# Kernel optimization log

Measured on AMD Instinct MI355X. Metric: run time of the kernel, lower is better.

The kernel has to match this reference:

```python
import jax, jax.numpy as jnp
import numpy as np

KEY_DIM = 1024
SCALE = KEY_DIM ** -0.5


def setup_inputs() -> dict:
    key = jax.random.key(0)
    k1, k2, k3, k4 = jax.random.split(key, 4)
    B, S, E = 4, 2048, 1024
    x = jax.random.normal(k1, (B, S, E), dtype=jnp.float32)
    WQ = jax.random.normal(k2, (KEY_DIM, E), dtype=jnp.float32) * (E ** -0.5)
    WK = jax.random.normal(k3, (KEY_DIM, E), dtype=jnp.float32) * (E ** -0.5)
    WV = jax.random.normal(k4, (KEY_DIM, E), dtype=jnp.float32) * (E ** -0.5)
    return {"x": x, "WQ": WQ, "WK": WK, "WV": WV}


def reference(x, WQ, WK, WV):
    # x: [B, S, E]; Linear(bias=False) weights are [out, in] as in torch.
    q = jnp.einsum('bse,ke->bsk', x, WQ)   # [B, S, K]
    k = jnp.einsum('bse,ke->bsk', x, WK)   # [B, S, K]
    v = jnp.einsum('bse,ve->bsv', x, WV)   # [B, S, V]
    scores = jnp.einsum('bsk,btk->bst', q, k) * SCALE  # [B, S, S]
    # Faithful to torch: mask where tril(scores) == 0 (upper triangle).
    masked = jnp.where(jnp.tril(scores) == 0, -jnp.inf, scores)
    attn = jax.nn.softmax(masked, axis=-1)
    return jnp.einsum('bst,btv->bsv', attn, v)  # dropout=0.0 -> identity
```

## Files before the change

kernel.cpp:

```cpp
#include <hip/hip_runtime.h>

typedef _Float16 f16x8 __attribute__((ext_vector_type(8)));
typedef unsigned short u16x8v __attribute__((ext_vector_type(8)));
typedef unsigned short u16x4v __attribute__((ext_vector_type(4)));
typedef float f32x4 __attribute__((ext_vector_type(4)));

constexpr int SEQ = 2048;
constexpr int DIM = 1024;
constexpr int BATCH = 4;
constexpr size_t NBS = (size_t)BATCH * SEQ * DIM;

static __device__ __forceinline__ unsigned short f2h(float f) {
    return __builtin_bit_cast(unsigned short, (_Float16)f);
}
static __device__ __forceinline__ float h2f(unsigned short u) {
    return (float)__builtin_bit_cast(_Float16, u);
}
static __device__ __forceinline__ f16x8 ldsld(const unsigned short* p) {
    return __builtin_bit_cast(f16x8, *(const u16x8v*)p);
}
static __device__ __forceinline__ void gld_lds16(const unsigned short* g, unsigned short* l) {
    __builtin_amdgcn_global_load_lds(
        (const __attribute__((address_space(1))) void*)g,
        (__attribute__((address_space(3))) void*)l, 16, 0, 0);
}

__global__ __launch_bounds__(256) void cvt_all(
    const float* __restrict__ X,
    const float* __restrict__ W0, const float* __restrict__ W1,
    const float* __restrict__ W2,
    unsigned short* __restrict__ Xf, unsigned short* __restrict__ Wf)
{
    const int b = blockIdx.x;
    const float* src;
    unsigned short* dst;
    int i;
    if (b < 8192) {
        src = X; dst = Xf;
        i = b * 256 + threadIdx.x;
    } else {
        const int wb = b - 8192;
        const int z = wb >> 10;
        src = (z == 0) ? W0 : (z == 1) ? W1 : W2;
        dst = Wf + (size_t)z * DIM * DIM;
        i = (wb & 1023) * 256 + threadIdx.x;
    }
    float4 f = ((const float4*)src)[i];
    u16x4v h;
    h.x = f2h(f.x); h.y = f2h(f.y); h.z = f2h(f.z); h.w = f2h(f.w);
    ((u16x4v*)dst)[i] = h;
}


__global__ __launch_bounds__(256) void qkv_gemm(
    const unsigned short* __restrict__ Xf, const unsigned short* __restrict__ Wf,
    unsigned short* __restrict__ Qf, unsigned short* __restrict__ Kf,
    unsigned short* __restrict__ Vt)
{
    __shared__ __attribute__((aligned(16))) unsigned short Ah[128 * 64];
    __shared__ __attribute__((aligned(16))) unsigned short Bh[128 * 64];
    const int m0 = blockIdx.x * 128, n0 = blockIdx.y * 128, z = blockIdx.z;
    const unsigned short* Wz = Wf + (size_t)z * DIM * DIM;
    const int tid = threadIdx.x;
    const int w = tid >> 6, lane = tid & 63, q = lane >> 4, c = lane & 15;
    const int wrow = (w >> 1) * 64, wcol = (w & 1) * 64;
    const int g8 = lane >> 3;
    const int cu = (lane & 7) ^ g8;
    const int srow = w * 8 + g8;
    const int scol = cu * 8;
    unsigned short* lA = Ah + w * 512;
    unsigned short* lB = Bh + w * 512;
    const int c7 = c & 7;

    f32x4 acc[4][4];
#pragma unroll
    for (int a = 0; a < 4; ++a)
#pragma unroll
        for (int b = 0; b < 4; ++b) acc[a][b] = (f32x4){0.f, 0.f, 0.f, 0.f};

    for (int k0 = 0; k0 < DIM; k0 += 64) {
        __syncthreads();
        {
            const size_t ga = (size_t)(m0 + srow) * DIM + k0 + scol;
            const size_t gb = (size_t)(n0 + srow) * DIM + k0 + scol;
#pragma unroll
            for (int j = 0; j < 4; ++j) {
                gld_lds16(Xf + ga + (size_t)(j * 32) * DIM, lA + j * 2048);
                gld_lds16(Wz + gb + (size_t)(j * 32) * DIM, lB + j * 2048);
            }
        }
        __syncthreads();
#pragma unroll
        for (int kk = 0; kk < 2; ++kk) {
            f16x8 ah[4], bh[4];
#pragma unroll
            for (int mi = 0; mi < 4; ++mi)
                ah[mi] = ldsld(Ah + (wrow + mi * 16 + c) * 64 + (((kk << 2) + q) ^ c7) * 8);
#pragma unroll
            for (int ni = 0; ni < 4; ++ni)
                bh[ni] = ldsld(Bh + (wcol + ni * 16 + c) * 64 + (((kk << 2) + q) ^ c7) * 8);
#pragma unroll
            for (int mi = 0; mi < 4; ++mi)
#pragma unroll
                for (int ni = 0; ni < 4; ++ni)
                    acc[mi][ni] = __builtin_amdgcn_mfma_f32_16x16x32_f16(ah[mi], bh[ni], acc[mi][ni], 0, 0, 0);
        }
    }

    if (z == 2) {
#pragma unroll
        for (int mi = 0; mi < 4; ++mi) {
            const int mg = m0 + wrow + mi * 16 + q * 4;
            const int bb = mg >> 11, ss = mg & (SEQ - 1);
#pragma unroll
            for (int ni = 0; ni < 4; ++ni) {
                const int col = n0 + wcol + ni * 16 + c;
                u16x4v v;
                v.x = f2h(acc[mi][ni][0]);
                v.y = f2h(acc[mi][ni][1]);
                v.z = f2h(acc[mi][ni][2]);
                v.w = f2h(acc[mi][ni][3]);
                *(u16x4v*)(Vt + ((size_t)bb * DIM + col) * SEQ + ss) = v;
            }
        }
    } else {
        unsigned short* OH = z ? Kf : Qf;
#pragma unroll
        for (int mi = 0; mi < 4; ++mi)
#pragma unroll
            for (int ni = 0; ni < 4; ++ni) {
                const int col = n0 + wcol + ni * 16 + c;
#pragma unroll
                for (int r = 0; r < 4; ++r) {
                    const int row = m0 + wrow + mi * 16 + q * 4 + r;
                    OH[(size_t)row * DIM + col] = f2h(acc[mi][ni][r]);
                }
            }
    }
}

__global__ __launch_bounds__(256) void scores_gemm1b(
    const unsigned short* __restrict__ Q, const unsigned short* __restrict__ K,
    unsigned short* __restrict__ S)
{
    if (blockIdx.y > blockIdx.x) return;
    __shared__ __attribute__((aligned(16))) unsigned short Ah[128 * 64];
    __shared__ __attribute__((aligned(16))) unsigned short Bh[128 * 64];
    const int i0 = blockIdx.x * 128, j0 = blockIdx.y * 128, b = blockIdx.z;
    const unsigned short* Qb = Q + (size_t)b * SEQ * DIM;
    const unsigned short* Kb = K + (size_t)b * SEQ * DIM;
    unsigned short* Sb = S + (size_t)b * SEQ * SEQ;
    const int tid = threadIdx.x;
    const int w = tid >> 6, lane = tid & 63, q = lane >> 4, c = lane & 15;
    const int wrow = (w >> 1) * 64, wcol = (w & 1) * 64;
    const int g8 = lane >> 3;
    const int cu = (lane & 7) ^ g8;
    const int srow = w * 8 + g8;
    const int scol = cu * 8;
    unsigned short* lA = Ah + w * 512;
    unsigned short* lB = Bh + w * 512;
    const int c7 = c & 7;

    f32x4 acc[4][4];
#pragma unroll
    for (int a = 0; a < 4; ++a)
#pragma unroll
        for (int bq = 0; bq < 4; ++bq) acc[a][bq] = (f32x4){0.f, 0.f, 0.f, 0.f};

    for (int k0 = 0; k0 < DIM; k0 += 64) {
        __syncthreads();
        {
            const size_t ga = (size_t)(i0 + srow) * DIM + k0 + scol;
            const size_t gb = (size_t)(j0 + srow) * DIM + k0 + scol;
#pragma unroll
            for (int j = 0; j < 4; ++j) {
                gld_lds16(Qb + ga + (size_t)(j * 32) * DIM, lA + j * 2048);
                gld_lds16(Kb + gb + (size_t)(j * 32) * DIM, lB + j * 2048);
            }
        }
        __syncthreads();
#pragma unroll
        for (int kk = 0; kk < 2; ++kk) {
            f16x8 ah[4], bh[4];
#pragma unroll
            for (int mi = 0; mi < 4; ++mi)
                ah[mi] = ldsld(Ah + (wrow + mi * 16 + c) * 64 + (((kk << 2) + q) ^ c7) * 8);
#pragma unroll
            for (int ni = 0; ni < 4; ++ni)
                bh[ni] = ldsld(Bh + (wcol + ni * 16 + c) * 64 + (((kk << 2) + q) ^ c7) * 8);
#pragma unroll
            for (int mi = 0; mi < 4; ++mi)
#pragma unroll
                for (int ni = 0; ni < 4; ++ni)
                    acc[mi][ni] = __builtin_amdgcn_mfma_f32_16x16x32_f16(ah[mi], bh[ni], acc[mi][ni], 0, 0, 0);
        }
    }
#pragma unroll
    for (int mi = 0; mi < 4; ++mi)
#pragma unroll
        for (int ni = 0; ni < 4; ++ni) {
            const int col = j0 + wcol + ni * 16 + c;
#pragma unroll
            for (int r = 0; r < 4; ++r) {
                const int row = i0 + wrow + mi * 16 + q * 4 + r;
                const float sc = acc[mi][ni][r] * 0.03125f;
                Sb[(size_t)row * SEQ + col] =
                    (sc == 0.f) ? (unsigned short)0xFC00u : f2h(sc);
            }
        }
}

__global__ __launch_bounds__(256) void softmax_row_b(
    const unsigned short* __restrict__ S, unsigned short* __restrict__ P)
{
    const int i = blockIdx.x, t = threadIdx.x;
    const size_t ro = ((size_t)blockIdx.y * SEQ + i) * SEQ;
    const int wid = t >> 6, lane = t & 63;
    __shared__ float redm[4], reds[4];
    const int j0 = t * 8;
    const int rti = (i & ~127) + 128;
    float sv[8];
    float mx = -__builtin_inff();
    if (j0 <= i) {
        u16x8v raw = *(const u16x8v*)(S + ro + j0);
#pragma unroll
        for (int u = 0; u < 8; ++u) {
            float s = (j0 + u <= i) ? h2f(raw[u]) : -__builtin_inff();
            sv[u] = s;
            mx = fmaxf(mx, s);
        }
    } else {
#pragma unroll
        for (int u = 0; u < 8; ++u) sv[u] = -__builtin_inff();
    }
#pragma unroll
    for (int off = 1; off < 64; off <<= 1) mx = fmaxf(mx, __shfl_xor(mx, off));
    if (lane == 0) redm[wid] = mx;
    __syncthreads();
    const float M = fmaxf(fmaxf(redm[0], redm[1]), fmaxf(redm[2], redm[3]));
    float sum = 0.f;
#pragma unroll
    for (int u = 0; u < 8; ++u) {
        float e = __expf(sv[u] - M);
        sv[u] = e;
        sum += e;
    }
#pragma unroll
    for (int off = 1; off < 64; off <<= 1) sum += __shfl_xor(sum, off);
    if (lane == 0) reds[wid] = sum;
    __syncthreads();
    const float rinv = 1.f / (reds[0] + reds[1] + reds[2] + reds[3]);
    if (j0 < rti) {
        u16x8v o;
#pragma unroll
        for (int u = 0; u < 8; ++u) o[u] = f2h(sv[u] * rinv);
        *(u16x8v*)(P + ro + j0) = o;
    }
}

__global__ __launch_bounds__(256) void pv_gemm(
    const unsigned short* __restrict__ Pm, const unsigned short* __restrict__ Vt,
    float* __restrict__ Out)
{
    __shared__ __attribute__((aligned(16))) unsigned short Ps[128 * 64];
    __shared__ __attribute__((aligned(16))) unsigned short Vs[128 * 64];
    const int i0 = blockIdx.x * 128, d0 = blockIdx.y * 128, b = blockIdx.z;
    const int tid = threadIdx.x;
    const int w = tid >> 6, lane = tid & 63, q = lane >> 4, c = lane & 15;
    const int wrow = (w >> 1) * 64, wcol = (w & 1) * 64;
    const int g8 = lane >> 3;
    const int cu = (lane & 7) ^ g8;
    const int srow = w * 8 + g8;
    const int scol = cu * 8;
    unsigned short* lA = Ps + w * 512;
    unsigned short* lB = Vs + w * 512;
    const int c7 = c & 7;

    f32x4 acc[4][4];
#pragma unroll
    for (int a = 0; a < 4; ++a)
#pragma unroll
        for (int bq = 0; bq < 4; ++bq) acc[a][bq] = (f32x4){0.f, 0.f, 0.f, 0.f};

    const int njs = i0 / 64 + 2;

    for (int ks = 0; ks < njs; ++ks) {
        const int j0 = ks * 64;
        __syncthreads();
        {
            const size_t gpa = ((size_t)b * SEQ + i0 + srow) * SEQ + j0 + scol;
            const size_t gva = ((size_t)b * DIM + d0 + srow) * SEQ + j0 + scol;
#pragma unroll
            for (int j = 0; j < 4; ++j) {
                gld_lds16(Pm + gpa + (size_t)(j * 32) * SEQ, lA + j * 2048);
                gld_lds16(Vt + gva + (size_t)(j * 32) * SEQ, lB + j * 2048);
            }
        }
        __syncthreads();
#pragma unroll
        for (int kk = 0; kk < 2; ++kk) {
            f16x8 ah[4], bh[4];
#pragma unroll
            for (int mi = 0; mi < 4; ++mi)
                ah[mi] = ldsld(Ps + (wrow + mi * 16 + c) * 64 + (((kk << 2) + q) ^ c7) * 8);
#pragma unroll
            for (int ni = 0; ni < 4; ++ni)
                bh[ni] = ldsld(Vs + (wcol + ni * 16 + c) * 64 + (((kk << 2) + q) ^ c7) * 8);
#pragma unroll
            for (int mi = 0; mi < 4; ++mi)
#pragma unroll
                for (int ni = 0; ni < 4; ++ni)
                    acc[mi][ni] = __builtin_amdgcn_mfma_f32_16x16x32_f16(ah[mi], bh[ni], acc[mi][ni], 0, 0, 0);
        }
    }
#pragma unroll
    for (int mi = 0; mi < 4; ++mi)
#pragma unroll
        for (int ni = 0; ni < 4; ++ni) {
            const int dcol = d0 + wcol + ni * 16 + c;
#pragma unroll
            for (int r = 0; r < 4; ++r) {
                const int i = i0 + wrow + mi * 16 + q * 4 + r;
                Out[((size_t)b * SEQ + i) * DIM + dcol] = acc[mi][ni][r];
            }
        }
}

extern "C" void kernel_launch(void* const* d_in, const int* in_sizes, int n_in,
                              void* d_out, int out_size, void* d_ws, size_t ws_size,
                              hipStream_t stream)
{
    (void)out_size; (void)ws_size;
    const float* X = nullptr;
    const float* Wv[3] = {nullptr, nullptr, nullptr};
    int nw = 0;
    for (int i = 0; i < n_in; ++i) {
        if (in_sizes[i] == (int)NBS)
            X = (const float*)d_in[i];
        else if (nw < 3)
            Wv[nw++] = (const float*)d_in[i];
    }

    unsigned short* ws = (unsigned short*)d_ws;
    unsigned short* Qf = ws;
    unsigned short* Kf = ws + NBS;
    unsigned short* Vt = ws + 2 * NBS;
    unsigned short* Xf = ws + 3 * NBS;
    unsigned short* Pp = ws + 3 * NBS;
    unsigned short* Sb = ws + 5 * NBS;
    unsigned short* Wf = ws + 7 * NBS;
    float* Out = (float*)d_out;

    cvt_all<<<dim3(8192 + 3072), 256, 0, stream>>>(X, Wv[0], Wv[1], Wv[2], Xf, Wf);

    qkv_gemm<<<dim3(64, 8, 3), 256, 0, stream>>>(Xf, Wf, Qf, Kf, Vt);

    scores_gemm1b<<<dim3(16, 16, BATCH), 256, 0, stream>>>(Qf, Kf, Sb);
    softmax_row_b<<<dim3(SEQ, BATCH), 256, 0, stream>>>(Sb, Pp);

    pv_gemm<<<dim3(16, 8, BATCH), 256, 0, stream>>>(Pp, Vt, Out);
}
```

Before: 243.1 us.

## Split-K long causal PV tiles with atomics and remap QKV blocks across XCDs

The PV GEMM now divides each of the eight longest causal row tiles into two K-range halves that accumulate into the output with float atomicAdd, while short tiles still store directly. This evens out per-block work in the triangular PV workload, at the cost of zeroing the output with a memset and doing atomic traffic. The QKV GEMM is launched on a flat 1D grid with a swizzled block index so that neighbouring tiles, including the three weight matrices for the same M/N tile, land on the same XCD to improve L2 reuse.

```diff
diff --git a/kernel.cpp b/kernel.cpp
--- a/kernel.cpp
+++ b/kernel.cpp
@@ -51,7 +51,6 @@
     ((u16x4v*)dst)[i] = h;
 }
 
-
 __global__ __launch_bounds__(256) void qkv_gemm(
     const unsigned short* __restrict__ Xf, const unsigned short* __restrict__ Wf,
     unsigned short* __restrict__ Qf, unsigned short* __restrict__ Kf,
@@ -59,7 +58,13 @@
 {
     __shared__ __attribute__((aligned(16))) unsigned short Ah[128 * 64];
     __shared__ __attribute__((aligned(16))) unsigned short Bh[128 * 64];
-    const int m0 = blockIdx.x * 128, n0 = blockIdx.y * 128, z = blockIdx.z;
+    const int flat = blockIdx.x;
+    const int wgid = (flat & 7) * 192 + (flat >> 3);
+    const int mt = wgid / 24;
+    const int rem = wgid - mt * 24;
+    const int nt = rem / 3;
+    const int z = rem - nt * 3;
+    const int m0 = mt * 128, n0 = nt * 128;
     const unsigned short* Wz = Wf + (size_t)z * DIM * DIM;
     const int tid = threadIdx.x;
     const int w = tid >> 6, lane = tid & 63, q = lane >> 4, c = lane & 15;
@@ -264,7 +269,20 @@
 {
     __shared__ __attribute__((aligned(16))) unsigned short Ps[128 * 64];
     __shared__ __attribute__((aligned(16))) unsigned short Vs[128 * 64];
-    const int i0 = blockIdx.x * 128, d0 = blockIdx.y * 128, b = blockIdx.z;
+    const int xt = blockIdx.x;
+    int i0t, ks0, ks1;
+    bool useAtomic;
+    if (xt < 8) {
+        i0t = xt; ks0 = 0; ks1 = 2 * xt + 2; useAtomic = false;
+    } else {
+        i0t = 8 + ((xt - 8) >> 1);
+        const int njs = 2 * i0t + 2;
+        const int nh = i0t + 1;
+        const int s = (xt - 8) & 1;
+        ks0 = s ? nh : 0; ks1 = s ? njs : nh;
+        useAtomic = true;
+    }
+    const int i0 = i0t * 128, d0 = blockIdx.y * 128, b = blockIdx.z;
     const int tid = threadIdx.x;
     const int w = tid >> 6, lane = tid & 63, q = lane >> 4, c = lane & 15;
     const int wrow = (w >> 1) * 64, wcol = (w & 1) * 64;
@@ -282,9 +300,7 @@
 #pragma unroll
         for (int bq = 0; bq < 4; ++bq) acc[a][bq] = (f32x4){0.f, 0.f, 0.f, 0.f};
 
-    const int njs = i0 / 64 + 2;
-
-    for (int ks = 0; ks < njs; ++ks) {
+    for (int ks = ks0; ks < ks1; ++ks) {
         const int j0 = ks * 64;
         __syncthreads();
         {
@@ -321,7 +337,9 @@
 #pragma unroll
             for (int r = 0; r < 4; ++r) {
                 const int i = i0 + wrow + mi * 16 + q * 4 + r;
-                Out[((size_t)b * SEQ + i) * DIM + dcol] = acc[mi][ni][r];
+                float* p = &Out[((size_t)b * SEQ + i) * DIM + dcol];
+                if (useAtomic) atomicAdd(p, acc[mi][ni][r]);
+                else *p = acc[mi][ni][r];
             }
         }
 }
@@ -353,10 +371,11 @@
 
     cvt_all<<<dim3(8192 + 3072), 256, 0, stream>>>(X, Wv[0], Wv[1], Wv[2], Xf, Wf);
 
-    qkv_gemm<<<dim3(64, 8, 3), 256, 0, stream>>>(Xf, Wf, Qf, Kf, Vt);
+    qkv_gemm<<<dim3(1536), 256, 0, stream>>>(Xf, Wf, Qf, Kf, Vt);
 
     scores_gemm1b<<<dim3(16, 16, BATCH), 256, 0, stream>>>(Qf, Kf, Sb);
     softmax_row_b<<<dim3(SEQ, BATCH), 256, 0, stream>>>(Sb, Pp);
 
-    pv_gemm<<<dim3(16, 8, BATCH), 256, 0, stream>>>(Pp, Vt, Out);
-}
+    hipMemsetAsync(d_out, 0, (size_t)BATCH * SEQ * DIM * sizeof(float), stream);
+    pv_gemm<<<dim3(24, 8, BATCH), 256, 0, stream>>>(Pp, Vt, Out);
+}
```

Result: slower. 253.2 us (+4.2%).
